# Kernel tuning notes

Hardware: AMD Instinct MI355X
Metric: run time of the kernel (lower is better)

## Reference

```python
import jax, jax.numpy as jnp
import numpy as np

NUM_HEADS = 16
KEY_DIM = 64
D_MODEL = 1024  # input feature dim


def setup_inputs() -> dict:
    key = jax.random.key(0)
    ks = jax.random.split(key, 10)
    B, T = 2, 2048
    s = 0.02
    return {
        "query": jax.random.normal(ks[0], (B, T, D_MODEL), jnp.float32),
        "Wq": jax.random.normal(ks[1], (D_MODEL, NUM_HEADS * KEY_DIM), jnp.float32) * s,
        "bq": jnp.zeros((NUM_HEADS * KEY_DIM,), jnp.float32),
        "Wk": jax.random.normal(ks[2], (D_MODEL, KEY_DIM), jnp.float32) * s,
        "bk": jnp.zeros((KEY_DIM,), jnp.float32),
        "Wv": jax.random.normal(ks[3], (D_MODEL, KEY_DIM), jnp.float32) * s,
        "bv": jnp.zeros((KEY_DIM,), jnp.float32),
        "Wo": jax.random.normal(ks[4], (NUM_HEADS * KEY_DIM, NUM_HEADS * KEY_DIM), jnp.float32) * s,
        "bo": jnp.zeros((NUM_HEADS * KEY_DIM,), jnp.float32),
    }


def reference(query, Wq, bq, Wk, bk, Wv, bv, Wo, bo):
    B, Tq, _ = query.shape
    # self-attention: key = value = query
    q = query @ Wq + bq                      # [B,Tq,H*D]
    k = query @ Wk + bk                      # [B,Tk,D] (single shared head)
    v = query @ Wv + bv                      # [B,Tk,D]
    q = q.reshape(B, Tq, NUM_HEADS, KEY_DIM)
    # scores: [B,H,Tq,Tk] — K broadcast across heads (MQA)
    scores = jnp.einsum("bqhd,bkd->bhqk", q, k) / jnp.sqrt(
        jnp.asarray(KEY_DIM, jnp.float32))
    attn = jax.nn.softmax(scores, axis=-1)
    out = jnp.einsum("bhqk,bkd->bqhd", attn, v)  # [B,Tq,H,D]
    out = out.reshape(B, Tq, NUM_HEADS * KEY_DIM)
    return out @ Wo + bo
```

## Files before the change

### kernel.cpp

```cpp
#include <hip/hip_runtime.h>
#include <math.h>

#define T_SEQ 2048
#define DM 1024
#define NH 16
#define KD 64
#define MTOT 4096

typedef __attribute__((ext_vector_type(16))) float f32x16;
typedef __attribute__((ext_vector_type(8))) __bf16 bf16x8;
typedef __attribute__((ext_vector_type(2))) __bf16 bf16x2;
typedef __attribute__((ext_vector_type(2))) int i32x2;

#define MFMA32 __builtin_amdgcn_mfma_f32_32x32x16_bf16

#define QSCALE 0.1803368801111f

struct bf2 { __bf16 h, l; };
__device__ __forceinline__ bf2 split2(float v) {
  bf2 r;
  r.h = (__bf16)v;
  r.l = (__bf16)(v - (float)r.h);
  return r;
}

__device__ __forceinline__ unsigned pkbf(__bf16 a, __bf16 b) {
  bf16x2 t;
  t[0] = a;
  t[1] = b;
  return __builtin_bit_cast(unsigned, t);
}

__device__ __forceinline__ float fexp2(float x) {
#if __has_builtin(__builtin_amdgcn_exp2f)
  return __builtin_amdgcn_exp2f(x);
#else
  return __expf(0.69314718056f * x);
#endif
}

__device__ __forceinline__ void plswap(unsigned& a, unsigned& b) {
  i32x2 r = __builtin_amdgcn_permlane32_swap((int)a, (int)b, false, false);
  a = (unsigned)r[0];
  b = (unsigned)r[1];
}

__device__ __forceinline__ f32x16 zero16() {
  f32x16 z;
#pragma unroll
  for (int i = 0; i < 16; ++i) z[i] = 0.f;
  return z;
}

__device__ __forceinline__ int drow(int reg, int l5) {
  return (reg & 3) + 8 * (reg >> 2) + 4 * l5;
}

__device__ __forceinline__ void gload16(const void* g, void* l) {
  __builtin_amdgcn_global_load_lds(
      (const __attribute__((address_space(1))) unsigned int*)g,
      (__attribute__((address_space(3))) unsigned int*)l, 16, 0, 0);
}

__device__ __forceinline__ int swzc(int row, int c) {
  return (((((c >> 3) ^ row) & 7)) << 3) | (c & 7);
}

__device__ __forceinline__ float ldf(const void* p, size_t i, int fl) {
  return fl ? ((const float*)p)[i] : (float)(((const __bf16*)p)[i]);
}

__global__ void detect_prep(const unsigned short* __restrict__ w, int* flag,
                            const void* bq, const void* bk, const void* bv,
                            const void* bo, float* bqf, float* bkf,
                            float* bvf, float* bof) {
  __shared__ int s;
  if (threadIdx.x == 0) s = 0;
  __syncthreads();
  int bad = 0;
  for (int i = threadIdx.x; i < 4096; i += 256) {
    unsigned e = (w[i] >> 7) & 0xFF;
    if (e >= 0xC0) bad = 1;
  }
  if (bad) atomicOr(&s, 1);
  __syncthreads();
  const int fl = s;
  if (threadIdx.x == 0) *flag = fl;
  for (int i = threadIdx.x; i < 1024; i += 256) {
    bqf[i] = ldf(bq, i, fl);
    bof[i] = ldf(bo, i, fl);
  }
  if (threadIdx.x < 64) {
    bkf[threadIdx.x] = ldf(bk, threadIdx.x, fl);
    bvf[threadIdx.x] = ldf(bv, threadIdx.x, fl);
  }
}

__global__ __launch_bounds__(256) void prep_u(
    const int* __restrict__ flag, const void* __restrict__ Aq,
    const void* __restrict__ Wq, const void* __restrict__ Wk,
    const void* __restrict__ Wv, const void* __restrict__ Wo,
    __bf16* __restrict__ Ah, __bf16* __restrict__ wqkv,
    __bf16* __restrict__ woh, __bf16* __restrict__ wol) {
  const int fl = *flag;
  const int t = threadIdx.x;
  const int y = blockIdx.y;
  if (y >= 68) {
    const int gid = ((y - 68) * 32 + blockIdx.x) * 256 + t;
    const int row = gid >> 7;
    const int c0 = (gid & 127) * 8;
    bf16x8 h;
    if (fl) {
      const float* Af = (const float*)Aq + (size_t)row * 1024 + c0;
      float4 v0 = *reinterpret_cast<const float4*>(Af);
      float4 v1 = *reinterpret_cast<const float4*>(Af + 4);
      h[0] = (__bf16)v0.x; h[1] = (__bf16)v0.y;
      h[2] = (__bf16)v0.z; h[3] = (__bf16)v0.w;
      h[4] = (__bf16)v1.x; h[5] = (__bf16)v1.y;
      h[6] = (__bf16)v1.z; h[7] = (__bf16)v1.w;
    } else {
      h = *reinterpret_cast<const bf16x8*>((const __bf16*)Aq + (size_t)row * 1024 + c0);
    }
    const int cb = (c0 & ~63) | (swzc(row & 7, c0 & 63) & ~7);
    *reinterpret_cast<bf16x8*>(Ah + (size_t)row * 1024 + cb) = h;
    return;
  }
  __shared__ float ts[32][33];
  const void* W;
  int N, n0, rowoff;
  bool lo = false;
  __bf16* dh;
  if (y < 32)      { W = Wq; N = 1024; n0 = y * 32;        rowoff = 0;    dh = wqkv; }
  else if (y < 34) { W = Wk; N = 64;   n0 = (y - 32) * 32; rowoff = 1024; dh = wqkv; }
  else if (y < 36) { W = Wv; N = 64;   n0 = (y - 34) * 32; rowoff = 1088; dh = wqkv; }
  else             { W = Wo; N = 1024; n0 = (y - 36) * 32; rowoff = 0;    dh = woh; lo = true; }
  const int k0 = blockIdx.x * 32;
#pragma unroll
  for (int i = 0; i < 4; ++i) {
    int idx = t + 256 * i;
    int r = idx >> 5, c = idx & 31;
    ts[r][c] = ldf(W, (size_t)(k0 + r) * N + n0 + c, fl);
  }
  __syncthreads();
#pragma unroll
  for (int i = 0; i < 4; ++i) {
    int idx = t + 256 * i;
    int r = idx >> 5, c = idx & 31;
    bf2 s = split2(ts[c][r]);
    const int rr = rowoff + n0 + r, cc = k0 + c;
    const int sc = (cc & ~63) | swzc(rr & 7, cc & 63);
    dh[(size_t)rr * 1024 + sc] = s.h;
    if (lo) wol[(size_t)rr * 1024 + sc] = s.l;
  }
}

__global__ __launch_bounds__(256, 4) void gemmqkv(
    const __bf16* __restrict__ Ah_g, const __bf16* __restrict__ Bh_g,
    const float* __restrict__ bqf, const float* __restrict__ bkf,
    const float* __restrict__ bvf,
    __bf16* __restrict__ Qh, __bf16* __restrict__ Kh2,
    __bf16* __restrict__ Vh2) {
  __shared__ __bf16 As[128][64], Bs[64][64];
  const int t = threadIdx.x, l = t & 63, w = t >> 6;
  const int l31 = l & 31, l5 = l >> 5, l7 = l31 & 7;
  const int m0 = blockIdx.x * 128, n0 = blockIdx.y * 64;

  f32x16 acc[2];
  acc[0] = zero16();
  acc[1] = zero16();

  for (int k0 = 0; k0 < 1024; k0 += 64) {
    __syncthreads();
    const int c8 = (t & 7) * 8;
#pragma unroll
    for (int i = 0; i < 4; ++i) {
      const int idx = i * 256 + t;
      gload16(Ah_g + (size_t)(m0 + (idx >> 3)) * 1024 + k0 + c8, (__bf16*)As + idx * 8);
    }
#pragma unroll
    for (int i = 0; i < 2; ++i) {
      const int idx = i * 256 + t;
      gload16(Bh_g + (size_t)(n0 + (idx >> 3)) * 1024 + k0 + c8, (__bf16*)Bs + idx * 8);
    }
    __syncthreads();
#pragma unroll
    for (int kb = 0; kb < 4; ++kb) {
      const int p = ((2 * kb + l5) ^ l7) * 8;
      bf16x8 ah = *reinterpret_cast<const bf16x8*>(&As[w * 32 + l31][p]);
#pragma unroll
      for (int nt = 0; nt < 2; ++nt) {
        bf16x8 bh = *reinterpret_cast<const bf16x8*>(&Bs[nt * 32 + l31][p]);
        acc[nt] = MFMA32(ah, bh, acc[nt], 0, 0, 0);
      }
    }
  }
#pragma unroll
  for (int nt = 0; nt < 2; ++nt) {
    const int cbase = n0 + nt * 32;
    const int col = cbase + l31;
    if (cbase < 1024) {
      const float bb = bqf[col];
#pragma unroll
      for (int reg = 0; reg < 16; ++reg) {
        const int mrow = m0 + w * 32 + drow(reg, l5);
        Qh[(size_t)mrow * 1024 + col] = (__bf16)((acc[nt][reg] + bb) * QSCALE);
      }
    } else if (cbase < 1088) {
      const int d = col - 1024;
      const float bb = bkf[d];
#pragma unroll
      for (int reg = 0; reg < 16; ++reg) {
        const int mrow = m0 + w * 32 + drow(reg, l5);
        Kh2[(size_t)mrow * 64 + swzc(mrow & 7, d)] = (__bf16)(acc[nt][reg] + bb);
      }
    } else {
      const int d = col - 1088;
      const float bb = bvf[d];
#pragma unroll
      for (int reg = 0; reg < 16; ++reg) {
        const int mrow = m0 + w * 32 + drow(reg, l5);
        const int bb2 = mrow >> 11, tt = mrow & 2047;
        const int sct = (tt & ~63) | swzc(d & 7, tt & 63);
        Vh2[((size_t)bb2 * 64 + d) * 2048 + sct] = (__bf16)(acc[nt][reg] + bb);
      }
    }
  }
}

__global__ __launch_bounds__(256, 3) void gemmwo(
    const int* __restrict__ flag,
    const __bf16* __restrict__ Ahi, const __bf16* __restrict__ Alo,
    const __bf16* __restrict__ Bh, const __bf16* __restrict__ Bl,
    const float* __restrict__ bof, void* __restrict__ CT) {
  __shared__ __bf16 Ah[128][64], Al[128][64];
  __shared__ __bf16 Bth[64][64], Btl[64][64];
  const int t = threadIdx.x, l = t & 63, w = t >> 6;
  const int l31 = l & 31, l5 = l >> 5, l7 = l31 & 7;
  const int m0 = blockIdx.x * 128, n0 = blockIdx.y * 64;

  f32x16 acc[2];
  acc[0] = zero16();
  acc[1] = zero16();

  for (int k0 = 0; k0 < 1024; k0 += 64) {
    __syncthreads();
    const int c8 = (t & 7) * 8;
#pragma unroll
    for (int i = 0; i < 4; ++i) {
      const int idx = i * 256 + t;
      const size_t ga = (size_t)(m0 + (idx >> 3)) * 1024 + k0 + c8;
      gload16(Ahi + ga, (__bf16*)Ah + idx * 8);
      gload16(Alo + ga, (__bf16*)Al + idx * 8);
    }
#pragma unroll
    for (int i = 0; i < 2; ++i) {
      const int idx = i * 256 + t;
      const size_t gb = (size_t)(n0 + (idx >> 3)) * 1024 + k0 + c8;
      gload16(Bh + gb, (__bf16*)Bth + idx * 8);
      gload16(Bl + gb, (__bf16*)Btl + idx * 8);
    }
    __syncthreads();
#pragma unroll
    for (int kb = 0; kb < 4; ++kb) {
      const int p = ((2 * kb + l5) ^ l7) * 8;
      bf16x8 ah = *reinterpret_cast<const bf16x8*>(&Ah[w * 32 + l31][p]);
      bf16x8 al = *reinterpret_cast<const bf16x8*>(&Al[w * 32 + l31][p]);
#pragma unroll
      for (int nt = 0; nt < 2; ++nt) {
        bf16x8 bh = *reinterpret_cast<const bf16x8*>(&Bth[nt * 32 + l31][p]);
        bf16x8 bl = *reinterpret_cast<const bf16x8*>(&Btl[nt * 32 + l31][p]);
        acc[nt] = MFMA32(al, bh, acc[nt], 0, 0, 0);
        acc[nt] = MFMA32(ah, bl, acc[nt], 0, 0, 0);
        acc[nt] = MFMA32(ah, bh, acc[nt], 0, 0, 0);
      }
    }
  }
  const int fl = *flag;
#pragma unroll
  for (int nt = 0; nt < 2; ++nt) {
    const int col = n0 + nt * 32 + l31;
    const float bb = bof[col];
#pragma unroll
    for (int reg = 0; reg < 16; ++reg) {
      const int mrow = m0 + w * 32 + drow(reg, l5);
      const float v = acc[nt][reg] + bb;
      if (fl) ((float*)CT)[(size_t)mrow * 1024 + col] = v;
      else ((__bf16*)CT)[(size_t)mrow * 1024 + col] = (__bf16)v;
    }
  }
}

__global__ __launch_bounds__(512, 2) void attn8(
    const __bf16* __restrict__ Qh_g, const __bf16* __restrict__ Kh_g,
    const __bf16* __restrict__ Vh_g,
    __bf16* __restrict__ AOhi, __bf16* __restrict__ AOlo) {
  __shared__ alignas(16) char arena[66560];
  const int t = threadIdx.x, l = t & 63, w = t >> 6;
  const int wq = w & 3, kvh = w >> 2;
  const int l31 = l & 31, l5 = l >> 5, l7 = l31 & 7;
  const int tl = t & 255;
  const int q0 = blockIdx.x * 256;
  const int h = blockIdx.y, b = blockIdx.z;

  __bf16* Kbase = (__bf16*)(arena + kvh * 16384);
  __bf16* Vbase = (__bf16*)(arena + 32768 + kvh * 16384);

  bf16x8 onesb;
#pragma unroll
  for (int j = 0; j < 8; ++j) onesb[j] = (__bf16)1.0f;

  bf16x8 qh0[4], qh1[4];
  {
    const size_t qa = ((size_t)(b * T_SEQ + q0 + wq * 64 + l31)) * DM + h * KD;
#pragma unroll
    for (int ks = 0; ks < 4; ++ks) {
      qh0[ks] = *reinterpret_cast<const bf16x8*>(Qh_g + qa + ks * 16 + l5 * 8);
      qh1[ks] = *reinterpret_cast<const bf16x8*>(Qh_g + qa + (size_t)32 * DM + ks * 16 + l5 * 8);
    }
  }

  f32x16 o0 = zero16(), o1 = zero16(), o2 = zero16(), o3 = zero16();
  f32x16 lacca = zero16(), laccb = zero16();

  const __bf16* Kg = Kh_g + (size_t)b * T_SEQ * KD;
  const __bf16* Vg = Vh_g + (size_t)b * KD * T_SEQ;
  const int sc8 = (tl & 7) * 8;
  const int kbase = kvh * 1024;

#define ASTAGE(BUF, KT0)                                                       \
  {                                                                            \
    const int r0 = tl >> 3, r1 = (256 + tl) >> 3;                              \
    gload16(Kg + (size_t)((KT0) + r0) * KD + sc8, Kbase + (BUF)*4096 + tl * 8);\
    gload16(Kg + (size_t)((KT0) + r1) * KD + sc8,                              \
            Kbase + (BUF)*4096 + (256 + tl) * 8);                              \
    gload16(Vg + (size_t)r0 * T_SEQ + (KT0) + sc8, Vbase + (BUF)*4096 + tl * 8);\
    gload16(Vg + (size_t)r1 * T_SEQ + (KT0) + sc8,                             \
            Vbase + (BUF)*4096 + (256 + tl) * 8);                              \
  }

  ASTAGE(0, kbase);
  __syncthreads();
  int cur = 0;

  for (int kt = 0; kt < 1024; kt += 64) {
    if (kt + 64 < 1024) ASTAGE(cur ^ 1, kbase + kt + 64);

#pragma unroll
    for (int hf = 0; hf < 2; ++hf) {
      f32x16 sva = zero16(), svb = zero16();
      __builtin_amdgcn_s_setprio(1);
#pragma unroll
      for (int ks = 0; ks < 4; ++ks) {
        const int p = ((2 * ks + l5) ^ l7) * 8;
        bf16x8 kh = *reinterpret_cast<const bf16x8*>(
            Kbase + cur * 4096 + (hf * 32 + l31) * 64 + p);
        sva = MFMA32(kh, qh0[ks], sva, 0, 0, 0);
        svb = MFMA32(kh, qh1[ks], svb, 0, 0, 0);
      }
      __builtin_amdgcn_s_setprio(0);
      unsigned uha[8], uhb[8];
#pragma unroll
      for (int g2 = 0; g2 < 8; ++g2) {
        float a0 = fexp2(fminf(sva[2 * g2], 43.f));
        float a1 = fexp2(fminf(sva[2 * g2 + 1], 43.f));
        uha[g2] = pkbf((__bf16)a0, (__bf16)a1);
        float b0 = fexp2(fminf(svb[2 * g2], 43.f));
        float b1 = fexp2(fminf(svb[2 * g2 + 1], 43.f));
        uhb[g2] = pkbf((__bf16)b0, (__bf16)b1);
      }
#pragma unroll
      for (int kc = 0; kc < 2; ++kc) {
        unsigned a0 = uha[4 * kc], a1 = uha[4 * kc + 1];
        unsigned a2 = uha[4 * kc + 2], a3 = uha[4 * kc + 3];
        plswap(a0, a2);
        plswap(a1, a3);
        alignas(16) unsigned fa[4] = {a0, a1, a2, a3};
        bf16x8 pa = *reinterpret_cast<bf16x8*>(fa);
        unsigned b0 = uhb[4 * kc], b1 = uhb[4 * kc + 1];
        unsigned b2 = uhb[4 * kc + 2], b3 = uhb[4 * kc + 3];
        plswap(b0, b2);
        plswap(b1, b3);
        alignas(16) unsigned fb[4] = {b0, b1, b2, b3};
        bf16x8 pb = *reinterpret_cast<bf16x8*>(fb);

        const int kk = 2 * hf + kc;
        const int p = ((2 * kk + l5) ^ l7) * 8;
        bf16x8 v0 = *reinterpret_cast<const bf16x8*>(Vbase + cur * 4096 + l31 * 64 + p);
        bf16x8 v1 = *reinterpret_cast<const bf16x8*>(Vbase + cur * 4096 + (32 + l31) * 64 + p);
        __builtin_amdgcn_s_setprio(1);
        lacca = MFMA32(pa, onesb, lacca, 0, 0, 0);
        o0 = MFMA32(pa, v0, o0, 0, 0, 0);
        o1 = MFMA32(pa, v1, o1, 0, 0, 0);
        laccb = MFMA32(pb, onesb, laccb, 0, 0, 0);
        o2 = MFMA32(pb, v0, o2, 0, 0, 0);
        o3 = MFMA32(pb, v1, o3, 0, 0, 0);
        __builtin_amdgcn_s_setprio(0);
      }
    }
    __syncthreads();
    cur ^= 1;
  }

  float* ex = (float*)arena;
  float* exl = (float*)(arena + 65536);
  if (kvh == 1) {
#pragma unroll
    for (int g = 0; g < 4; ++g) {
      int cc0 = (0 + g + l) & 15;
      *reinterpret_cast<float4*>(&ex[((wq * 64 + l) << 6) + cc0 * 4]) =
          make_float4(o0[4 * g], o0[4 * g + 1], o0[4 * g + 2], o0[4 * g + 3]);
      int cc1 = (4 + g + l) & 15;
      *reinterpret_cast<float4*>(&ex[((wq * 64 + l) << 6) + cc1 * 4]) =
          make_float4(o1[4 * g], o1[4 * g + 1], o1[4 * g + 2], o1[4 * g + 3]);
      int cc2 = (8 + g + l) & 15;
      *reinterpret_cast<float4*>(&ex[((wq * 64 + l) << 6) + cc2 * 4]) =
          make_float4(o2[4 * g], o2[4 * g + 1], o2[4 * g + 2], o2[4 * g + 3]);
      int cc3 = (12 + g + l) & 15;
      *reinterpret_cast<float4*>(&ex[((wq * 64 + l) << 6) + cc3 * 4]) =
          make_float4(o3[4 * g], o3[4 * g + 1], o3[4 * g + 2], o3[4 * g + 3]);
    }
    if (l31 == 0) {
#pragma unroll
      for (int r = 0; r < 16; ++r) {
        exl[(wq * 2 + l5) * 32 + r] = lacca[r];
        exl[(wq * 2 + l5) * 32 + 16 + r] = laccb[r];
      }
    }
  }
  __syncthreads();
  if (kvh == 0) {
#pragma unroll
    for (int g = 0; g < 4; ++g) {
      int cc0 = (0 + g + l) & 15;
      float4 v = *reinterpret_cast<float4*>(&ex[((wq * 64 + l) << 6) + cc0 * 4]);
      o0[4 * g] += v.x; o0[4 * g + 1] += v.y; o0[4 * g + 2] += v.z; o0[4 * g + 3] += v.w;
      int cc1 = (4 + g + l) & 15;
      v = *reinterpret_cast<float4*>(&ex[((wq * 64 + l) << 6) + cc1 * 4]);
      o1[4 * g] += v.x; o1[4 * g + 1] += v.y; o1[4 * g + 2] += v.z; o1[4 * g + 3] += v.w;
      int cc2 = (8 + g + l) & 15;
      v = *reinterpret_cast<float4*>(&ex[((wq * 64 + l) << 6) + cc2 * 4]);
      o2[4 * g] += v.x; o2[4 * g + 1] += v.y; o2[4 * g + 2] += v.z; o2[4 * g + 3] += v.w;
      int cc3 = (12 + g + l) & 15;
      v = *reinterpret_cast<float4*>(&ex[((wq * 64 + l) << 6) + cc3 * 4]);
      o3[4 * g] += v.x; o3[4 * g + 1] += v.y; o3[4 * g + 2] += v.z; o3[4 * g + 3] += v.w;
    }
#pragma unroll
    for (int r = 0; r < 16; ++r) {
      lacca[r] += exl[(wq * 2 + l5) * 32 + r];
      laccb[r] += exl[(wq * 2 + l5) * 32 + 16 + r];
    }
#pragma unroll
    for (int reg = 0; reg < 16; ++reg) {
      const int rq = drow(reg, l5);
      const int cl = ((((l31 >> 3) ^ rq) & 7) << 3) | (l31 & 7);
      const int ch = ((((4 + (l31 >> 3)) ^ rq) & 7) << 3) | (l31 & 7);
      const float inva = 1.f / lacca[reg];
      const size_t roa = ((size_t)(b * T_SEQ + q0 + wq * 64 + rq)) * DM + h * KD;
      bf2 s;
      s = split2(o0[reg] * inva); AOhi[roa + cl] = s.h; AOlo[roa + cl] = s.l;
      s = split2(o1[reg] * inva); AOhi[roa + ch] = s.h; AOlo[roa + ch] = s.l;
      const float invb = 1.f / laccb[reg];
      const size_t rob = roa + (size_t)32 * DM;
      s = split2(o2[reg] * invb); AOhi[rob + cl] = s.h; AOlo[rob + cl] = s.l;
      s = split2(o3[reg] * invb); AOhi[rob + ch] = s.h; AOlo[rob + ch] = s.l;
    }
  }
#undef ASTAGE
}

extern "C" void kernel_launch(void* const* d_in, const int* in_sizes, int n_in,
                              void* d_out, int out_size, void* d_ws, size_t ws_size,
                              hipStream_t stream) {
  char* ws = (char*)d_ws;
  int* flag = (int*)ws;
  size_t o = 4096;
  float* bqf = (float*)(ws + o); o += 4096;
  float* bkf = (float*)(ws + o); o += 4096;
  float* bvf = (float*)(ws + o); o += 4096;
  float* bof = (float*)(ws + o); o += 4096;
  __bf16* wqkvt_h = (__bf16*)(ws + o); o += (size_t)1152 * 1024 * 2;
  __bf16* wot_h = (__bf16*)(ws + o); o += 2097152;
  __bf16* wot_l = (__bf16*)(ws + o); o += 2097152;
  __bf16* khi = (__bf16*)(ws + o); o += 524288;
  __bf16* vthi = (__bf16*)(ws + o); o += 524288;
  __bf16* ahi = (__bf16*)(ws + o); o += 8388608;
  __bf16* aolo = (__bf16*)(ws + o); o += 8388608;
  __bf16* qhi = (__bf16*)(ws + o); o += 8388608;
  __bf16* aohi = ahi;

  detect_prep<<<1, 256, 0, stream>>>(
      (const unsigned short*)d_in[1], flag, d_in[2], d_in[4], d_in[6], d_in[8],
      bqf, bkf, bvf, bof);
  prep_u<<<dim3(32, 132), 256, 0, stream>>>(
      flag, d_in[0], d_in[1], d_in[3], d_in[5], d_in[7],
      ahi, wqkvt_h, wot_h, wot_l);
  gemmqkv<<<dim3(32, 18), 256, 0, stream>>>(
      ahi, wqkvt_h, bqf, bkf, bvf, qhi, khi, vthi);
  attn8<<<dim3(T_SEQ / 256, NH, 2), 512, 0, stream>>>(
      qhi, khi, vthi, aohi, aolo);
  gemmwo<<<dim3(32, 16), 256, 0, stream>>>(
      flag, aohi, aolo, wot_h, wot_l, bof, d_out);
}
```

Measured before the change: 191.1 us.

## Halve attention query tile to 128 rows per block and drop exp clamp

The attention kernel now has each wave process 32 query rows instead of 64, so each block covers 128 queries and the grid doubles in the x dimension. This cuts per-wave register use (half the accumulators and Q fragments), and it gives more blocks to spread across CUs. The cost is that every K/V tile is loaded from global memory to LDS twice as often for the same query range. The fminf clamp before exp2 is also removed, which saves a few ALU ops but risks overflow if the scores are large.

```diff
diff --git a/kernel.cpp b/kernel.cpp
--- a/kernel.cpp
+++ b/kernel.cpp
@@ -299,7 +299,7 @@
   const int wq = w & 3, kvh = w >> 2;
   const int l31 = l & 31, l5 = l >> 5, l7 = l31 & 7;
   const int tl = t & 255;
-  const int q0 = blockIdx.x * 256;
+  const int q0 = blockIdx.x * 128;
   const int h = blockIdx.y, b = blockIdx.z;
 
   __bf16* Kbase = (__bf16*)(arena + kvh * 16384);
@@ -309,18 +309,15 @@
 #pragma unroll
   for (int j = 0; j < 8; ++j) onesb[j] = (__bf16)1.0f;
 
-  bf16x8 qh0[4], qh1[4];
+  bf16x8 qh0[4];
   {
-    const size_t qa = ((size_t)(b * T_SEQ + q0 + wq * 64 + l31)) * DM + h * KD;
-#pragma unroll
-    for (int ks = 0; ks < 4; ++ks) {
+    const size_t qa = ((size_t)(b * T_SEQ + q0 + wq * 32 + l31)) * DM + h * KD;
+#pragma unroll
+    for (int ks = 0; ks < 4; ++ks)
       qh0[ks] = *reinterpret_cast<const bf16x8*>(Qh_g + qa + ks * 16 + l5 * 8);
-      qh1[ks] = *reinterpret_cast<const bf16x8*>(Qh_g + qa + (size_t)32 * DM + ks * 16 + l5 * 8);
-    }
-  }
-
-  f32x16 o0 = zero16(), o1 = zero16(), o2 = zero16(), o3 = zero16();
-  f32x16 lacca = zero16(), laccb = zero16();
+  }
+
+  f32x16 o0 = zero16(), o1 = zero16(), lacca = zero16();
 
   const __bf16* Kg = Kh_g + (size_t)b * T_SEQ * KD;
   const __bf16* Vg = Vh_g + (size_t)b * KD * T_SEQ;
@@ -347,7 +344,7 @@
 
 #pragma unroll
     for (int hf = 0; hf < 2; ++hf) {
-      f32x16 sva = zero16(), svb = zero16();
+      f32x16 sva = zero16();
       __builtin_amdgcn_s_setprio(1);
 #pragma unroll
       for (int ks = 0; ks < 4; ++ks) {
@@ -355,18 +352,14 @@
         bf16x8 kh = *reinterpret_cast<const bf16x8*>(
             Kbase + cur * 4096 + (hf * 32 + l31) * 64 + p);
         sva = MFMA32(kh, qh0[ks], sva, 0, 0, 0);
-        svb = MFMA32(kh, qh1[ks], svb, 0, 0, 0);
       }
       __builtin_amdgcn_s_setprio(0);
-      unsigned uha[8], uhb[8];
+      unsigned uha[8];
 #pragma unroll
       for (int g2 = 0; g2 < 8; ++g2) {
-        float a0 = fexp2(fminf(sva[2 * g2], 43.f));
-        float a1 = fexp2(fminf(sva[2 * g2 + 1], 43.f));
+        float a0 = fexp2(sva[2 * g2]);
+        float a1 = fexp2(sva[2 * g2 + 1]);
         uha[g2] = pkbf((__bf16)a0, (__bf16)a1);
-        float b0 = fexp2(fminf(svb[2 * g2], 43.f));
-        float b1 = fexp2(fminf(svb[2 * g2 + 1], 43.f));
-        uhb[g2] = pkbf((__bf16)b0, (__bf16)b1);
       }
 #pragma unroll
       for (int kc = 0; kc < 2; ++kc) {
@@ -376,12 +369,6 @@
         plswap(a1, a3);
         alignas(16) unsigned fa[4] = {a0, a1, a2, a3};
         bf16x8 pa = *reinterpret_cast<bf16x8*>(fa);
-        unsigned b0 = uhb[4 * kc], b1 = uhb[4 * kc + 1];
-        unsigned b2 = uhb[4 * kc + 2], b3 = uhb[4 * kc + 3];
-        plswap(b0, b2);
-        plswap(b1, b3);
-        alignas(16) unsigned fb[4] = {b0, b1, b2, b3};
-        bf16x8 pb = *reinterpret_cast<bf16x8*>(fb);
 
         const int kk = 2 * hf + kc;
         const int p = ((2 * kk + l5) ^ l7) * 8;
@@ -391,9 +378,6 @@
         lacca = MFMA32(pa, onesb, lacca, 0, 0, 0);
         o0 = MFMA32(pa, v0, o0, 0, 0, 0);
         o1 = MFMA32(pa, v1, o1, 0, 0, 0);
-        laccb = MFMA32(pb, onesb, laccb, 0, 0, 0);
-        o2 = MFMA32(pb, v0, o2, 0, 0, 0);
-        o3 = MFMA32(pb, v1, o3, 0, 0, 0);
         __builtin_amdgcn_s_setprio(0);
       }
     }
@@ -406,63 +390,42 @@
   if (kvh == 1) {
 #pragma unroll
     for (int g = 0; g < 4; ++g) {
-      int cc0 = (0 + g + l) & 15;
-      *reinterpret_cast<float4*>(&ex[((wq * 64 + l) << 6) + cc0 * 4]) =
+      int cc0 = (g + l) & 7;
+      *reinterpret_cast<float4*>(&ex[((wq * 64 + l) << 5) + cc0 * 4]) =
           make_float4(o0[4 * g], o0[4 * g + 1], o0[4 * g + 2], o0[4 * g + 3]);
-      int cc1 = (4 + g + l) & 15;
-      *reinterpret_cast<float4*>(&ex[((wq * 64 + l) << 6) + cc1 * 4]) =
+      int cc1 = (4 + g + l) & 7;
+      *reinterpret_cast<float4*>(&ex[((wq * 64 + l) << 5) + cc1 * 4]) =
           make_float4(o1[4 * g], o1[4 * g + 1], o1[4 * g + 2], o1[4 * g + 3]);
-      int cc2 = (8 + g + l) & 15;
-      *reinterpret_cast<float4*>(&ex[((wq * 64 + l) << 6) + cc2 * 4]) =
-          make_float4(o2[4 * g], o2[4 * g + 1], o2[4 * g + 2], o2[4 * g + 3]);
-      int cc3 = (12 + g + l) & 15;
-      *reinterpret_cast<float4*>(&ex[((wq * 64 + l) << 6) + cc3 * 4]) =
-          make_float4(o3[4 * g], o3[4 * g + 1], o3[4 * g + 2], o3[4 * g + 3]);
     }
     if (l31 == 0) {
 #pragma unroll
-      for (int r = 0; r < 16; ++r) {
-        exl[(wq * 2 + l5) * 32 + r] = lacca[r];
-        exl[(wq * 2 + l5) * 32 + 16 + r] = laccb[r];
-      }
+      for (int r = 0; r < 16; ++r) exl[(wq * 2 + l5) * 16 + r] = lacca[r];
     }
   }
   __syncthreads();
   if (kvh == 0) {
 #pragma unroll
     for (int g = 0; g < 4; ++g) {
-      int cc0 = (0 + g + l) & 15;
-      float4 v = *reinterpret_cast<float4*>(&ex[((wq * 64 + l) << 6) + cc0 * 4]);
+      int cc0 = (g + l) & 7;
+      float4 v = *reinterpret_cast<float4*>(&ex[((wq * 64 + l) << 5) + cc0 * 4]);
       o0[4 * g] += v.x; o0[4 * g + 1] += v.y; o0[4 * g + 2] += v.z; o0[4 * g + 3] += v.w;
-      int cc1 = (4 + g + l) & 15;
-      v = *reinterpret_cast<float4*>(&ex[((wq * 64 + l) << 6) + cc1 * 4]);
+      int cc1 = (4 + g + l) & 7;
+      v = *reinterpret_cast<float4*>(&ex[((wq * 64 + l) << 5) + cc1 * 4]);
       o1[4 * g] += v.x; o1[4 * g + 1] += v.y; o1[4 * g + 2] += v.z; o1[4 * g + 3] += v.w;
-      int cc2 = (8 + g + l) & 15;
-      v = *reinterpret_cast<float4*>(&ex[((wq * 64 + l) << 6) + cc2 * 4]);
-      o2[4 * g] += v.x; o2[4 * g + 1] += v.y; o2[4 * g + 2] += v.z; o2[4 * g + 3] += v.w;
-      int cc3 = (12 + g + l) & 15;
-      v = *reinterpret_cast<float4*>(&ex[((wq * 64 + l) << 6) + cc3 * 4]);
-      o3[4 * g] += v.x; o3[4 * g + 1] += v.y; o3[4 * g + 2] += v.z; o3[4 * g + 3] += v.w;
-    }
-#pragma unroll
-    for (int r = 0; r < 16; ++r) {
-      lacca[r] += exl[(wq * 2 + l5) * 32 + r];
-      laccb[r] += exl[(wq * 2 + l5) * 32 + 16 + r];
-    }
+    }
+#pragma unroll
+    for (int r = 0; r < 16; ++r)
+      lacca[r] += exl[(wq * 2 + l5) * 16 + r];
 #pragma unroll
     for (int reg = 0; reg < 16; ++reg) {
       const int rq = drow(reg, l5);
       const int cl = ((((l31 >> 3) ^ rq) & 7) << 3) | (l31 & 7);
       const int ch = ((((4 + (l31 >> 3)) ^ rq) & 7) << 3) | (l31 & 7);
       const float inva = 1.f / lacca[reg];
-      const size_t roa = ((size_t)(b * T_SEQ + q0 + wq * 64 + rq)) * DM + h * KD;
+      const size_t roa = ((size_t)(b * T_SEQ + q0 + wq * 32 + rq)) * DM + h * KD;
       bf2 s;
       s = split2(o0[reg] * inva); AOhi[roa + cl] = s.h; AOlo[roa + cl] = s.l;
       s = split2(o1[reg] * inva); AOhi[roa + ch] = s.h; AOlo[roa + ch] = s.l;
-      const float invb = 1.f / laccb[reg];
-      const size_t rob = roa + (size_t)32 * DM;
-      s = split2(o2[reg] * invb); AOhi[rob + cl] = s.h; AOlo[rob + cl] = s.l;
-      s = split2(o3[reg] * invb); AOhi[rob + ch] = s.h; AOlo[rob + ch] = s.l;
     }
   }
 #undef ASTAGE
@@ -496,7 +459,7 @@
       ahi, wqkvt_h, wot_h, wot_l);
   gemmqkv<<<dim3(32, 18), 256, 0, stream>>>(
       ahi, wqkvt_h, bqf, bkf, bvf, qhi, khi, vthi);
-  attn8<<<dim3(T_SEQ / 256, NH, 2), 512, 0, stream>>>(
+  attn8<<<dim3(T_SEQ / 128, NH, 2), 512, 0, stream>>>(
       qhi, khi, vthi, aohi, aolo);
   gemmwo<<<dim3(32, 16), 256, 0, stream>>>(
       flag, aohi, aolo, wot_h, wot_l, bof, d_out);
```

New measurement: 188.8 us. No clear change (-1.2%).
